# Kernel optimization log

Hardware: AMD Instinct MI355X
Metric: run time of the kernel (lower is better)

Reference implementation:

```python
import jax, jax.numpy as jnp
import numpy as np

B, N = 16, 1023            # batch, signal length
T = N + 1                  # frames: hop=1, gaussian centers 0..N
F_BINS = N + 1             # rfft(2N) -> N+1 frequency bins
HID, NCLS = 128, 10


def setup_inputs() -> dict:
    key = jax.random.key(0)
    k = jax.random.split(key, 3)
    x = jax.random.normal(k[0], (B, N), dtype=jnp.float32)
    lambd = jnp.asarray(32.0, dtype=jnp.float32)  # learnable window width (sigma)
    feat = F_BINS * T
    W1 = jax.random.normal(k[1], (HID, feat), dtype=jnp.float32) / np.float32(np.sqrt(feat))
    b1 = jnp.zeros((HID,), jnp.float32)
    W2 = jax.random.normal(k[2], (NCLS, HID), dtype=jnp.float32) / np.float32(np.sqrt(HID))
    b2 = jnp.zeros((NCLS,), jnp.float32)
    return {"x": x, "lambd": lambd, "W1": W1, "b1": b1, "W2": W2, "b2": b2}


def _spectrogram(x, lambd):
    """Whole-signal differentiable Gaussian spectrogram (non-optimized path, hop=1).

    S[b, f, t] = | sum_n (x[b,n]-mean) * exp(-0.5*((n-t)/|lambd|)^2) * e^{-2pi i f n / (2N)} |^2
    Vectorized over the batch (replaces the per-sample Python loop).
    """
    n = x.shape[-1]
    sigma = jnp.abs(lambd)
    t = jnp.arange(n, dtype=jnp.float32)
    tc = jnp.arange(n + 1, dtype=jnp.float32)  # frame centers 0..n (n//hop + 1 frames)
    win = jnp.exp(-0.5 * ((t[None, :] - tc[:, None]) / sigma) ** 2)  # [T, n]
    xc = x - jnp.mean(x, axis=-1, keepdims=True)                     # per-sample mean removal
    xw = xc[:, None, :] * win[None]                                  # [B, T, n]
    spec = jnp.abs(jnp.fft.rfft(xw, n=2 * n, axis=-1)) ** 2          # [B, T, n+1]
    return jnp.transpose(spec, (0, 2, 1))[:, None]                   # [B, 1, n+1, T]


def reference(x, lambd, W1, b1, W2, b2):
    s = _spectrogram(x, lambd)                       # [B, 1, F_BINS, T]
    flat = s.reshape(s.shape[0], -1)                 # [B, F_BINS*T]
    h = jax.nn.relu(flat @ W1.T + b1)                # fc1 + relu
    out = h @ W2.T + b2                              # fc2
    return out, s
```

## Files before the change

### kernel.cpp

```cpp
#include <hip/hip_runtime.h>
#include <math.h>

#define NSIG   1023
#define BATCH  16
#define FT     1024
#define KW     256
#define RHALF  128
#define XPAD   1280
#define HID    128

#define OFF_XCP  0u
#define OFF_G    20480u
#define OFF_HRAW 20736u
#define OFF_TAB  22784u
#define TAB_ECH  0u
#define TAB_ECL  262144u
#define TAB_ESH  524288u
#define TAB_ESL  786432u

typedef int    i32x4  __attribute__((ext_vector_type(4)));
typedef float  f32x4  __attribute__((ext_vector_type(4)));
typedef __bf16 bf16x8 __attribute__((ext_vector_type(8)));
typedef unsigned short u16;

static __device__ __forceinline__ unsigned bfbits(float v) {
    unsigned u = __builtin_bit_cast(unsigned, v);
    return (u + 0x7fffu + ((u >> 16) & 1u)) >> 16;
}

__global__ void k_prep(const float* __restrict__ x, float* __restrict__ ws) {
    int b = blockIdx.x;
    __shared__ float red[256];
    float s = 0.f;
    for (int i = threadIdx.x; i < NSIG; i += 256) s += x[b * NSIG + i];
    red[threadIdx.x] = s;
    __syncthreads();
    for (int o = 128; o > 0; o >>= 1) {
        if (threadIdx.x < o) red[threadIdx.x] += red[threadIdx.x + o];
        __syncthreads();
    }
    float mean = red[0] * (1.0f / NSIG);
    float* xcp = ws + OFF_XCP + b * XPAD;
    for (int i = threadIdx.x; i < XPAD; i += 256) {
        int n = i - RHALF;
        xcp[i] = (n >= 0 && n < NSIG) ? (x[b * NSIG + n] - mean) : 0.f;
    }
}

__global__ void k_tables(const float* __restrict__ lambd, float* __restrict__ ws) {
    int bid = blockIdx.x;
    if (bid == 1024) {
        float sigma = fabsf(lambd[0]);
        float inv2s2 = 0.5f / (sigma * sigma);
        for (int i = threadIdx.x; i < KW; i += 256) {
            float d = (float)(i - RHALF);
            ws[OFF_G + i] = expf(-d * d * inv2s2);
        }
        for (int i = threadIdx.x; i < 2048; i += 256) ws[OFF_HRAW + i] = 0.f;
        return;
    }
    int idx = bid * 256 + threadIdx.x;
    int f = idx >> 8, k = idx & 255;
    int d = k - RHALF;
    int p = f * d;
    int m = p % 2046; if (m < 0) m += 2046;
    double ang = (double)m * (6.283185307179586476925286766559 / 2046.0);
    double sv, cv;
    sincos(ang, &sv, &cv);
    float cf = (float)cv, sf = (float)sv;
    u16* tab = (u16*)(ws + OFF_TAB);
    unsigned chb = bfbits(cf);
    float chf = __builtin_bit_cast(float, chb << 16);
    unsigned clb = bfbits(cf - chf);
    unsigned shb = bfbits(sf);
    float shf = __builtin_bit_cast(float, shb << 16);
    unsigned slb = bfbits(sf - shf);
    tab[TAB_ECH + idx] = (u16)chb;
    tab[TAB_ECL + idx] = (u16)clb;
    tab[TAB_ESH + idx] = (u16)shb;
    tab[TAB_ESL + idx] = (u16)slb;
}

__global__ __launch_bounds__(512, 4) void k_spec(const float* __restrict__ ws,
                                                 float* __restrict__ out) {
    __shared__ u16 yH[64 * 256];
    __shared__ u16 yL[64 * 256];
    int t0 = blockIdx.x * 64, f0 = blockIdx.y * 128, b = blockIdx.z;
    int tid = threadIdx.x;
    int wave = tid >> 6, lane = tid & 63;
    int lo = lane & 15, hi4 = lane >> 4;
    const u16* tab = (const u16*)(ws + OFF_TAB);
    const float* xcp = ws + OFF_XCP + b * XPAD;
    const float* gw  = ws + OFF_G;

    #pragma unroll
    for (int i = 0; i < 4; i++) {
        int idx = tid + i * 512;
        int t = idx >> 5, kg = idx & 31;
        int k = kg * 8;
        const float* xp = xcp + t0 + t + k;
        float4 g0 = *(const float4*)&gw[k];
        float4 g1 = *(const float4*)&gw[k + 4];
        float yv[8];
        yv[0] = xp[0] * g0.x; yv[1] = xp[1] * g0.y;
        yv[2] = xp[2] * g0.z; yv[3] = xp[3] * g0.w;
        yv[4] = xp[4] * g1.x; yv[5] = xp[5] * g1.y;
        yv[6] = xp[6] * g1.z; yv[7] = xp[7] * g1.w;
        unsigned hb[8], lb[8];
        #pragma unroll
        for (int j = 0; j < 8; j++) {
            unsigned u = __builtin_bit_cast(unsigned, yv[j]);
            unsigned h = (u + 0x7fffu + ((u >> 16) & 1u)) & 0xffff0000u;
            float hf = __builtin_bit_cast(float, h);
            hb[j] = h >> 16;
            lb[j] = bfbits(yv[j] - hf);
        }
        i32x4 ph, pl;
        ph.x = (int)(hb[0] | (hb[1] << 16)); ph.y = (int)(hb[2] | (hb[3] << 16));
        ph.z = (int)(hb[4] | (hb[5] << 16)); ph.w = (int)(hb[6] | (hb[7] << 16));
        pl.x = (int)(lb[0] | (lb[1] << 16)); pl.y = (int)(lb[2] | (lb[3] << 16));
        pl.z = (int)(lb[4] | (lb[5] << 16)); pl.w = (int)(lb[6] | (lb[7] << 16));
        int wb = ((t * 512 + kg * 16) ^ ((t & 7) << 4));
        *(i32x4*)((char*)yH + wb) = ph;
        *(i32x4*)((char*)yL + wb) = pl;
    }
    __syncthreads();

    size_t arow = (size_t)(f0 + wave * 16 + lo) * 256 + hi4 * 8;
    const u16* pech = tab + TAB_ECH + arow;
    const u16* pecl = tab + TAB_ECL + arow;
    const u16* pesh = tab + TAB_ESH + arow;
    const u16* pesl = tab + TAB_ESL + arow;

    f32x4 reA[4], imA[4];
    #pragma unroll
    for (int i = 0; i < 4; i++) {
        reA[i] = (f32x4){0.f, 0.f, 0.f, 0.f};
        imA[i] = (f32x4){0.f, 0.f, 0.f, 0.f};
    }

    #pragma unroll 2
    for (int c = 0; c < 8; c++) {
        i32x4 ech = *(const i32x4*)(pech + c * 32);
        i32x4 ecl = *(const i32x4*)(pecl + c * 32);
        i32x4 esh = *(const i32x4*)(pesh + c * 32);
        i32x4 esl = *(const i32x4*)(pesl + c * 32);
        #pragma unroll
        for (int tt = 0; tt < 4; tt++) {
            int tr = tt * 16 + lo;
            int rb = ((tr * 512 + c * 64 + hi4 * 16) ^ ((tr & 7) << 4));
            i32x4 yh = *(const i32x4*)((const char*)yH + rb);
            i32x4 yl = *(const i32x4*)((const char*)yL + rb);
            asm("v_mfma_f32_16x16x32_bf16 %0, %1, %2, %0" : "+v"(reA[tt]) : "v"(ech), "v"(yh));
            asm("v_mfma_f32_16x16x32_bf16 %0, %1, %2, %0" : "+v"(imA[tt]) : "v"(esh), "v"(yh));
            asm("v_mfma_f32_16x16x32_bf16 %0, %1, %2, %0" : "+v"(reA[tt]) : "v"(ech), "v"(yl));
            asm("v_mfma_f32_16x16x32_bf16 %0, %1, %2, %0" : "+v"(imA[tt]) : "v"(esh), "v"(yl));
            asm("v_mfma_f32_16x16x32_bf16 %0, %1, %2, %0" : "+v"(reA[tt]) : "v"(ecl), "v"(yh));
            asm("v_mfma_f32_16x16x32_bf16 %0, %1, %2, %0" : "+v"(imA[tt]) : "v"(esl), "v"(yh));
        }
    }
    asm volatile("s_nop 7\n\ts_nop 7");

    float* dS = out + 160;
    #pragma unroll
    for (int tt = 0; tt < 4; tt++) {
        #pragma unroll
        for (int r = 0; r < 4; r++) {
            int f = f0 + wave * 16 + hi4 * 4 + r;
            float re = reA[tt][r], im = imA[tt][r];
            dS[((size_t)b << 20) + (size_t)f * 1024 + t0 + tt * 16 + lo] = re * re + im * im;
        }
    }
}

static __device__ __forceinline__ bf16x8 packc4(float4 a, float4 b) {
    bf16x8 r;
    r[0] = (__bf16)a.x; r[1] = (__bf16)a.y; r[2] = (__bf16)a.z; r[3] = (__bf16)a.w;
    r[4] = (__bf16)b.x; r[5] = (__bf16)b.y; r[6] = (__bf16)b.z; r[7] = (__bf16)b.w;
    return r;
}
static __device__ __forceinline__ bf16x8 packcv(f32x4 a, f32x4 b) {
    bf16x8 r;
    r[0] = (__bf16)a.x; r[1] = (__bf16)a.y; r[2] = (__bf16)a.z; r[3] = (__bf16)a.w;
    r[4] = (__bf16)b.x; r[5] = (__bf16)b.y; r[6] = (__bf16)b.z; r[7] = (__bf16)b.w;
    return r;
}

static __device__ __forceinline__ void stage8(const float* src0, float* dst, int sstep) {
    #pragma unroll
    for (int i = 0; i < 8; i++) {
        __builtin_amdgcn_global_load_lds(
            (const __attribute__((address_space(1))) void*)
                (src0 + (size_t)((i >> 1) * 16 + (i & 1) * 8) * (1u << 20) + (size_t)sstep * 32),
            (__attribute__((address_space(3))) void*)((char*)dst + i * 1024),
            16, 0, 0);
    }
}

__global__ __launch_bounds__(256, 2) void k_fc1(const float* __restrict__ S,
                                                const float* __restrict__ W1,
                                                float* __restrict__ hraw) {
    __shared__ float Wl[4][2][2048];
    int tid = threadIdx.x;
    int wave = tid >> 6, lane = tid & 63;
    int jg = wave >> 1;
    int ks = (blockIdx.x << 1) | (wave & 1);
    int bq = lane >> 4, lo = lane & 15;
    int rl = lane >> 3;
    int colf = ((lane & 7) ^ rl) << 2;

    const float* Sp = S + (size_t)lo * (1u << 20) + (size_t)ks * 512 + bq * 8;
    const float* src0 = W1 + (size_t)(jg * 64 + rl) * (1u << 20)
                      + (size_t)ks * 512 + colf;
    float* buf0 = &Wl[wave][0][0];
    float* buf1 = &Wl[wave][1][0];

    f32x4 acc[4];
    #pragma unroll
    for (int j = 0; j < 4; j++) acc[j] = (f32x4){0.f, 0.f, 0.f, 0.f};

    stage8(src0, buf0, 0);

    int sw = (lo & 7) << 4;
    int rbase0 = lo * 128 + bq * 32;

    #pragma unroll
    for (int s = 0; s < 16; s++) {
        const float* sp = Sp + s * 32;
        float4 a0 = *(const float4*)(sp);
        float4 a1 = *(const float4*)(sp + 4);
        if (s < 15) {
            stage8(src0, (s & 1) ? buf0 : buf1, s + 1);
            asm volatile("s_waitcnt vmcnt(8)" ::: "memory");
        } else {
            asm volatile("s_waitcnt vmcnt(2)" ::: "memory");
        }
        bf16x8 af = packc4(a0, a1);
        const char* wb = (const char*)((s & 1) ? buf1 : buf0);
        #pragma unroll
        for (int jt = 0; jt < 4; jt++) {
            f32x4 w0 = *(const f32x4*)(wb + jt * 2048 + ((rbase0) ^ sw));
            f32x4 w1 = *(const f32x4*)(wb + jt * 2048 + ((rbase0 + 16) ^ sw));
            acc[jt] = __builtin_amdgcn_mfma_f32_16x16x32_bf16(af, packcv(w0, w1),
                                                              acc[jt], 0, 0, 0);
        }
    }

    float* red = &Wl[wave][0][0];
    #pragma unroll
    for (int jt = 0; jt < 4; jt++) {
        #pragma unroll
        for (int r = 0; r < 4; r++) {
            red[(bq * 4 + r) * 64 + jt * 16 + lo] = acc[jt][r];
        }
    }
    __syncthreads();
    for (int p = tid; p < 2048; p += 256) {
        int g = p >> 10, idx = p & 1023;
        float v = Wl[g * 2][0][idx] + Wl[g * 2 + 1][0][idx];
        atomicAdd(&hraw[(idx >> 6) * HID + g * 64 + (idx & 63)], v);
    }
}

__global__ void k_head(const float* __restrict__ hraw, const float* __restrict__ b1,
                       const float* __restrict__ W2, const float* __restrict__ b2,
                       float* __restrict__ out) {
    __shared__ float hl[2048];
    int tid = threadIdx.x;
    for (int p = tid; p < 2048; p += 256) {
        float hv = hraw[p] + b1[p & 127];
        hl[p] = hv > 0.f ? hv : 0.f;
    }
    __syncthreads();
    if (tid < 160) {
        int b = tid / 10, c = tid - b * 10;
        float s = b2[c];
        for (int j = 0; j < 128; j++) s += hl[b * 128 + j] * W2[c * 128 + j];
        out[b * 10 + c] = s;
    }
}

extern "C" void kernel_launch(void* const* d_in, const int* in_sizes, int n_in,
                              void* d_out, int out_size, void* d_ws, size_t ws_size,
                              hipStream_t stream) {
    const float* x     = (const float*)d_in[0];
    const float* lambd = (const float*)d_in[1];
    const float* W1    = (const float*)d_in[2];
    const float* b1    = (const float*)d_in[3];
    const float* W2    = (const float*)d_in[4];
    const float* b2    = (const float*)d_in[5];
    float* out = (float*)d_out;
    float* ws  = (float*)d_ws;

    hipLaunchKernelGGL(k_prep,   dim3(16),         dim3(256), 0, stream, x, ws);
    hipLaunchKernelGGL(k_tables, dim3(1025),       dim3(256), 0, stream, lambd, ws);
    hipLaunchKernelGGL(k_spec,   dim3(16, 8, 16),  dim3(512), 0, stream, ws, out);
    hipLaunchKernelGGL(k_fc1,    dim3(1024),       dim3(256), 0, stream,
                       out + 160, W1, ws + OFF_HRAW);
    hipLaunchKernelGGL(k_head,   dim3(1),          dim3(256), 0, stream,
                       ws + OFF_HRAW, b1, W2, b2, out);
}
```

Baseline: 223.5 us.

## Retile fc1 so each block covers 16 hidden units across four k-slices

```diff
diff --git a/kernel.cpp b/kernel.cpp
--- a/kernel.cpp
+++ b/kernel.cpp
@@ -186,12 +186,15 @@
     return r;
 }
 
-static __device__ __forceinline__ void stage8(const float* src0, float* dst, int sstep) {
+static __device__ __forceinline__ void stageW(const float* base, float* dst,
+                                              int rowLane, int colb0) {
     #pragma unroll
     for (int i = 0; i < 8; i++) {
+        int sw = ((2 * (i & 3)) + rowLane) << 4;
+        const float* src = base + (size_t)(2 * i + rowLane) * (1u << 20)
+                         + ((colb0 ^ sw) >> 2);
         __builtin_amdgcn_global_load_lds(
-            (const __attribute__((address_space(1))) void*)
-                (src0 + (size_t)((i >> 1) * 16 + (i & 1) * 8) * (1u << 20) + (size_t)sstep * 32),
+            (const __attribute__((address_space(1))) void*)src,
             (__attribute__((address_space(3))) void*)((char*)dst + i * 1024),
             16, 0, 0);
     }
@@ -203,63 +206,55 @@
     __shared__ float Wl[4][2][2048];
     int tid = threadIdx.x;
     int wave = tid >> 6, lane = tid & 63;
-    int jg = wave >> 1;
-    int ks = (blockIdx.x << 1) | (wave & 1);
+    int jtg = blockIdx.x & 7;
+    int ksg = blockIdx.x >> 3;
+    int ks  = (ksg << 2) | wave;
     int bq = lane >> 4, lo = lane & 15;
-    int rl = lane >> 3;
-    int colf = ((lane & 7) ^ rl) << 2;
+    int rowLane = lane >> 5;
+    int colb0 = (lane & 31) << 4;
+    int sw = (lo & 7) << 4;
 
     const float* Sp = S + (size_t)lo * (1u << 20) + (size_t)ks * 512 + bq * 8;
-    const float* src0 = W1 + (size_t)(jg * 64 + rl) * (1u << 20)
-                      + (size_t)ks * 512 + colf;
+    const float* Wb = W1 + (size_t)(jtg * 16) * (1u << 20) + (size_t)ks * 512;
     float* buf0 = &Wl[wave][0][0];
     float* buf1 = &Wl[wave][1][0];
 
-    f32x4 acc[4];
-    #pragma unroll
-    for (int j = 0; j < 4; j++) acc[j] = (f32x4){0.f, 0.f, 0.f, 0.f};
-
-    stage8(src0, buf0, 0);
-
-    int sw = (lo & 7) << 4;
-    int rbase0 = lo * 128 + bq * 32;
-
-    #pragma unroll
-    for (int s = 0; s < 16; s++) {
-        const float* sp = Sp + s * 32;
-        float4 a0 = *(const float4*)(sp);
-        float4 a1 = *(const float4*)(sp + 4);
-        if (s < 15) {
-            stage8(src0, (s & 1) ? buf0 : buf1, s + 1);
+    f32x4 acc = {0.f, 0.f, 0.f, 0.f};
+
+    stageW(Wb, buf0, rowLane, colb0);
+
+    #pragma unroll
+    for (int s = 0; s < 4; s++) {
+        float4 sA0[4], sA1[4];
+        #pragma unroll
+        for (int c = 0; c < 4; c++) {
+            const float* sp = Sp + s * 128 + c * 32;
+            sA0[c] = *(const float4*)(sp);
+            sA1[c] = *(const float4*)(sp + 4);
+        }
+        if (s < 3) {
+            stageW(Wb + (s + 1) * 128, (s & 1) ? buf0 : buf1, rowLane, colb0);
             asm volatile("s_waitcnt vmcnt(8)" ::: "memory");
         } else {
-            asm volatile("s_waitcnt vmcnt(2)" ::: "memory");
-        }
-        bf16x8 af = packc4(a0, a1);
+            asm volatile("s_waitcnt vmcnt(0)" ::: "memory");
+        }
         const char* wb = (const char*)((s & 1) ? buf1 : buf0);
         #pragma unroll
-        for (int jt = 0; jt < 4; jt++) {
-            f32x4 w0 = *(const f32x4*)(wb + jt * 2048 + ((rbase0) ^ sw));
-            f32x4 w1 = *(const f32x4*)(wb + jt * 2048 + ((rbase0 + 16) ^ sw));
-            acc[jt] = __builtin_amdgcn_mfma_f32_16x16x32_bf16(af, packcv(w0, w1),
-                                                              acc[jt], 0, 0, 0);
+        for (int c = 0; c < 4; c++) {
+            f32x4 w0 = *(const f32x4*)(wb + lo * 512 + ((c * 128 + bq * 32) ^ sw));
+            f32x4 w1 = *(const f32x4*)(wb + lo * 512 + ((c * 128 + bq * 32 + 16) ^ sw));
+            acc = __builtin_amdgcn_mfma_f32_16x16x32_bf16(packc4(sA0[c], sA1[c]),
+                                                          packcv(w0, w1), acc, 0, 0, 0);
         }
     }
 
     float* red = &Wl[wave][0][0];
     #pragma unroll
-    for (int jt = 0; jt < 4; jt++) {
-        #pragma unroll
-        for (int r = 0; r < 4; r++) {
-            red[(bq * 4 + r) * 64 + jt * 16 + lo] = acc[jt][r];
-        }
-    }
-    __syncthreads();
-    for (int p = tid; p < 2048; p += 256) {
-        int g = p >> 10, idx = p & 1023;
-        float v = Wl[g * 2][0][idx] + Wl[g * 2 + 1][0][idx];
-        atomicAdd(&hraw[(idx >> 6) * HID + g * 64 + (idx & 63)], v);
-    }
+    for (int r = 0; r < 4; r++) red[(bq * 4 + r) * 16 + lo] = acc[r];
+    __syncthreads();
+    float v = Wl[0][0][tid & 255] + Wl[1][0][tid & 255]
+            + Wl[2][0][tid & 255] + Wl[3][0][tid & 255];
+    atomicAdd(&hraw[(tid >> 4) * HID + jtg * 16 + (tid & 15)], v);
 }
 
 __global__ void k_head(const float* __restrict__ hraw, const float* __restrict__ b1,
@@ -295,7 +290,7 @@
     hipLaunchKernelGGL(k_prep,   dim3(16),         dim3(256), 0, stream, x, ws);
     hipLaunchKernelGGL(k_tables, dim3(1025),       dim3(256), 0, stream, lambd, ws);
     hipLaunchKernelGGL(k_spec,   dim3(16, 8, 16),  dim3(512), 0, stream, ws, out);
-    hipLaunchKernelGGL(k_fc1,    dim3(1024),       dim3(256), 0, stream,
+    hipLaunchKernelGGL(k_fc1,    dim3(4096),       dim3(256), 0, stream,
                        out + 160, W1, ws + OFF_HRAW);
     hipLaunchKernelGGL(k_head,   dim3(1),          dim3(256), 0, stream,
                        ws + OFF_HRAW, b1, W2, b2, out);
```

Result: slower. 238.3 us (+6.6%).
